# Performance work log

Hardware: AMD Instinct MI355X
Metric: run time of the kernel (lower is better)

Reference implementation:

```python
import jax, jax.numpy as jnp
import numpy as np

BS, DEC, IN_LEN, HID, EMB, VOCAB = 16, 100, 512, 768, 768, 32000


def setup_inputs() -> dict:
    key = jax.random.key(0)
    ks = jax.random.split(key, 8)
    x = jax.random.normal(ks[0], (BS, DEC, HID), dtype=jnp.float32)
    attn_dist = jax.random.normal(ks[1], (BS, DEC, IN_LEN), dtype=jnp.float32)
    enc_input = jax.random.randint(ks[2], (BS, IN_LEN), 0, VOCAB, dtype=jnp.int32)
    enc_output = jax.random.normal(ks[3], (BS, IN_LEN, EMB), dtype=jnp.float32)
    # learned params
    W_vocab = jax.random.normal(ks[4], (HID, VOCAB), dtype=jnp.float32) / np.sqrt(HID)
    b_vocab = jnp.zeros((VOCAB,), dtype=jnp.float32)
    W_gen = jax.random.normal(ks[5], (HID + EMB, 1), dtype=jnp.float32) / np.sqrt(HID + EMB)
    b_gen = jnp.zeros((1,), dtype=jnp.float32)
    return {"x": x, "attn_dist": attn_dist, "enc_input": enc_input,
            "enc_output": enc_output, "W_vocab": W_vocab, "b_vocab": b_vocab,
            "W_gen": W_gen, "b_gen": b_gen}


def reference(x, attn_dist, enc_input, enc_output, W_vocab, b_vocab, W_gen, b_gen):
    # context vector: [bs, dec, emb] = attn @ enc_output
    context = jnp.einsum('bdl,ble->bde', attn_dist, enc_output)
    mix = jnp.concatenate([context, x], axis=2)              # [bs, dec, emb+hid]
    p_gen = jax.nn.sigmoid(mix @ W_gen + b_gen)              # [bs, dec, 1]
    logit = x @ W_vocab + b_vocab                            # [bs, dec, vocab]
    vocab_dist = jax.nn.softmax(logit, axis=2) * p_gen       # [bs, dec, vocab]
    attn_w = jax.nn.softmax(attn_dist, axis=2) * (1.0 - p_gen)  # [bs, dec, in_len]
    # scatter_add attention mass onto vocab ids (duplicate ids accumulate)
    b_idx = jnp.arange(BS)[:, None, None]
    d_idx = jnp.arange(DEC)[None, :, None]
    v_idx = enc_input[:, None, :]                            # broadcast over dec
    mixed = vocab_dist.at[b_idx, d_idx, v_idx].add(attn_w)
    return jnp.log(mixed)
```

## Files before the change

kernel.cpp:

```cpp
#include <hip/hip_runtime.h>
#include <math.h>

#define BS 16
#define DEC 100
#define IN_LEN 512
#define HID 768
#define EMB 768
#define VOCAB 32000
#define NROW (BS*DEC)
#define NTILE_M 13
#define NTILE_N2 125
#define KT2 24
#define A_SHORTS 4096
#define B_SHORTS 8192

using short8 = __attribute__((ext_vector_type(8))) short;
using ushort4v = __attribute__((ext_vector_type(4))) unsigned short;
using f32x4 = __attribute__((ext_vector_type(4))) float;

__device__ __forceinline__ unsigned short f2bf(float f) {
  unsigned u = __float_as_uint(f);
  u = u + 0x7FFFu + ((u >> 16) & 1u);
  return (unsigned short)(u >> 16);
}
__device__ __forceinline__ float bf2f(unsigned short h) {
  return __uint_as_float(((unsigned)h) << 16);
}

__device__ __forceinline__ void gll16(const void* g, void* l) {
  __builtin_amdgcn_global_load_lds(
      (const __attribute__((address_space(1))) unsigned int*)g,
      (__attribute__((address_space(3))) unsigned int*)l, 16, 0, 0);
}

__global__ __launch_bounds__(256) void k0_venc(const float* __restrict__ enc_out,
                                               const float* __restrict__ Wg,
                                               float* __restrict__ venc) {
  int row = blockIdx.x * 4 + (threadIdx.x >> 6);
  int lane = threadIdx.x & 63;
  const float* p = enc_out + (size_t)row * EMB;
  float s = 0.f;
  for (int e = lane; e < EMB; e += 64) s += p[e] * Wg[e];
  for (int off = 32; off; off >>= 1) s += __shfl_xor(s, off);
  if (lane == 0) venc[row] = s;
}

__global__ __launch_bounds__(256) void k1_row(const float* __restrict__ attn,
                                              const float* __restrict__ x,
                                              const float* __restrict__ venc,
                                              const float* __restrict__ Wg,
                                              const float* __restrict__ bgen,
                                              float* __restrict__ pg,
                                              float* __restrict__ lp,
                                              float* __restrict__ m_a,
                                              float* __restrict__ s_a) {
  int r = blockIdx.x;
  int b = r / DEC;
  int tid = threadIdx.x;
  const float* arow = attn + (size_t)r * IN_LEN;
  const float* ve = venc + b * IN_LEN;
  const float* xrow = x + (size_t)r * HID;

  float pdot = 0.f, m = -1e30f;
  for (int l = tid; l < IN_LEN; l += 256) { float a = arow[l]; pdot += a * ve[l]; m = fmaxf(m, a); }
  for (int h = tid; h < HID; h += 256) pdot += xrow[h] * Wg[HID + h];

  for (int off = 32; off; off >>= 1) pdot += __shfl_xor(pdot, off);
  for (int off = 32; off; off >>= 1) m = fmaxf(m, __shfl_xor(m, off));

  __shared__ float red[8];
  if ((tid & 63) == 0) { red[tid >> 6] = pdot; red[4 + (tid >> 6)] = m; }
  __syncthreads();
  float z = red[0] + red[1] + red[2] + red[3];
  m = fmaxf(fmaxf(red[4], red[5]), fmaxf(red[6], red[7]));

  float se = 0.f;
  for (int l = tid; l < IN_LEN; l += 256) se += expf(arow[l] - m);
  for (int off = 32; off; off >>= 1) se += __shfl_xor(se, off);
  __syncthreads();
  if ((tid & 63) == 0) red[tid >> 6] = se;
  __syncthreads();
  se = red[0] + red[1] + red[2] + red[3];

  if (tid == 0) {
    z += bgen[0];
    float p, l_p;
    if (z >= 0.f) { float e = expf(-z); p = 1.f / (1.f + e); l_p = -log1pf(e); }
    else          { float e = expf(z);  p = e / (1.f + e);   l_p = z - log1pf(e); }
    pg[r] = p; lp[r] = l_p; m_a[r] = m; s_a[r] = se;
  }
}

__global__ __launch_bounds__(256) void p0_pack_x(const float* __restrict__ X,
                                                 unsigned short* __restrict__ Xp) {
  int mtile = blockIdx.x, ks = blockIdx.y, tid = threadIdx.x;
  size_t base = ((size_t)(mtile * KT2 + ks)) * A_SHORTS;
#pragma unroll
  for (int i = 0; i < 2; i++) {
    int slot = tid + i * 256;
    int r = slot >> 2, s = slot & 3;
    int row = mtile * 128 + r;
    int k0 = ks * 32 + ((s ^ (r & 3)) << 3);
    short8 v;
    if (row < NROW) {
      const float* p = X + (size_t)row * HID + k0;
#pragma unroll
      for (int j = 0; j < 8; j++) v[j] = (short)f2bf(p[j]);
    } else {
#pragma unroll
      for (int j = 0; j < 8; j++) v[j] = 0;
    }
    *(short8*)&Xp[base + (size_t)slot * 8] = v;
  }
}

__global__ __launch_bounds__(256) void p0_pack_w(const float* __restrict__ W,
                                                 unsigned short* __restrict__ Wp) {
  __shared__ float ld[32][257];
  int ntile = blockIdx.x, ks = blockIdx.y, tid = threadIdx.x;
#pragma unroll
  for (int i = 0; i < 32; i++) {
    int idx = tid + i * 256;
    int kk = idx >> 8, nn = idx & 255;
    ld[kk][nn] = W[(size_t)(ks * 32 + kk) * VOCAB + ntile * 256 + nn];
  }
  __syncthreads();
  size_t base = ((size_t)(ntile * KT2 + ks)) * B_SHORTS;
#pragma unroll
  for (int i = 0; i < 4; i++) {
    int slot = tid + i * 256;
    int n = slot >> 2, s = slot & 3;
    int k0 = (s ^ (n & 3)) << 3;
    short8 v;
#pragma unroll
    for (int j = 0; j < 8; j++) v[j] = (short)f2bf(ld[k0 + j][n]);
    *(short8*)&Wp[base + (size_t)slot * 8] = v;
  }
}

__global__ __launch_bounds__(256, 2) void k2_gemm_v4(const unsigned short* __restrict__ Xp,
                                                     const unsigned short* __restrict__ Wp,
                                                     const float* __restrict__ bvocab,
                                                     float* __restrict__ out,
                                                     unsigned short* __restrict__ lbf,
                                                     float* __restrict__ part,
                                                     int use_bf) {
  __shared__ __align__(16) unsigned short sh[3][12288];

  int bid = blockIdx.x;
  const int NWG = NTILE_M * NTILE_N2;
  const int q = NWG / 8, rr = NWG % 8;
  int xcd = bid & 7, idx = bid >> 3;
  int wg = (xcd < rr ? xcd * (q + 1) : rr * (q + 1) + (xcd - rr) * q) + idx;
  int ntile = wg / NTILE_M, mtile = wg % NTILE_M;

  const int tid = threadIdx.x;
  const int wid = tid >> 6, lane = tid & 63;
  const int wr = wid >> 1, wc = wid & 1;
  const int l15 = lane & 15, hi = lane >> 4;
  const int phys = (hi ^ (l15 & 3)) * 8;

  const unsigned short* aSrc = Xp + (size_t)(mtile * KT2) * A_SHORTS;
  const unsigned short* bSrc = Wp + (size_t)(ntile * KT2) * B_SHORTS;

  const int aoff = (wr * 64 + l15) * 32 + phys;
  const int boff = (wc * 128 + l15) * 32 + phys;

  f32x4 acc[4][8] = {};

#pragma unroll
  for (int t = 0; t < 2; t++) {
    const unsigned short* a = aSrc + (size_t)t * A_SHORTS;
    const unsigned short* b = bSrc + (size_t)t * B_SHORTS;
    unsigned short* dA = &sh[t][0];
    unsigned short* dB = &sh[t][4096];
    gll16(a + (size_t)tid * 8,            dA + tid * 8);
    gll16(a + (size_t)(tid + 256) * 8,    dA + (tid + 256) * 8);
#pragma unroll
    for (int j2 = 0; j2 < 4; j2++)
      gll16(b + (size_t)(tid + j2 * 256) * 8, dB + (tid + j2 * 256) * 8);
  }
  asm volatile("s_waitcnt vmcnt(6)" ::: "memory");
  __builtin_amdgcn_s_barrier();
  asm volatile("" ::: "memory");

  int bcur = 0;
  for (int t = 0; t < KT2; ++t) {
    if (t + 2 < KT2) {
      int bn = bcur + 2; if (bn >= 3) bn -= 3;
      const unsigned short* a = aSrc + (size_t)(t + 2) * A_SHORTS;
      const unsigned short* b = bSrc + (size_t)(t + 2) * B_SHORTS;
      unsigned short* dA = &sh[bn][0];
      unsigned short* dB = &sh[bn][4096];
      gll16(a + (size_t)tid * 8,            dA + tid * 8);
      gll16(a + (size_t)(tid + 256) * 8,    dA + (tid + 256) * 8);
#pragma unroll
      for (int j2 = 0; j2 < 4; j2++)
        gll16(b + (size_t)(tid + j2 * 256) * 8, dB + (tid + j2 * 256) * 8);
    }
    const unsigned short* A = &sh[bcur][0];
    const unsigned short* B = &sh[bcur][4096];
    short8 af[4], bfr[8];
#pragma unroll
    for (int mm = 0; mm < 4; mm++) af[mm] = *(const short8*)&A[aoff + mm * 512];
#pragma unroll
    for (int nn = 0; nn < 8; nn++) bfr[nn] = *(const short8*)&B[boff + nn * 512];
    __builtin_amdgcn_s_setprio(1);
#pragma unroll
    for (int mm = 0; mm < 4; mm++)
#pragma unroll
      for (int nn = 0; nn < 8; nn++)
        acc[mm][nn] = __builtin_amdgcn_mfma_f32_16x16x32_bf16(af[mm], bfr[nn], acc[mm][nn], 0, 0, 0);
    __builtin_amdgcn_s_setprio(0);
    if (t < KT2 - 2) { asm volatile("s_waitcnt vmcnt(6)" ::: "memory"); }
    else             { asm volatile("s_waitcnt vmcnt(0)" ::: "memory"); }
    __builtin_amdgcn_s_barrier();
    asm volatile("" ::: "memory");
    bcur = bcur + 1; if (bcur >= 3) bcur = 0;
  }

  __syncthreads();

  float bb[8];
#pragma unroll
  for (int nn = 0; nn < 8; nn++) bb[nn] = bvocab[ntile * 256 + wc * 128 + nn * 16 + l15];
#pragma unroll
  for (int mm = 0; mm < 4; mm++)
#pragma unroll
    for (int nn = 0; nn < 8; nn++)
#pragma unroll
      for (int j = 0; j < 4; j++) acc[mm][nn][j] += bb[nn];

  unsigned short* ldsC = &sh[0][0];
  float* red = (float*)&sh[2][8192];

  if (use_bf) {
#pragma unroll
    for (int mm = 0; mm < 4; mm++) {
      int row0 = wr * 64 + mm * 16 + hi * 4;
#pragma unroll
      for (int nn = 0; nn < 8; nn++) {
        int col = wc * 128 + nn * 16 + l15;
#pragma unroll
        for (int j = 0; j < 4; j++) ldsC[(row0 + j) * 256 + col] = f2bf(acc[mm][nn][j]);
      }
    }
  } else {
#pragma unroll
    for (int mm = 0; mm < 4; mm++) {
      int row0 = mtile * 128 + wr * 64 + mm * 16 + hi * 4;
#pragma unroll
      for (int nn = 0; nn < 8; nn++) {
        int col = ntile * 256 + wc * 128 + nn * 16 + l15;
#pragma unroll
        for (int j = 0; j < 4; j++) {
          int row = row0 + j;
          if (row < NROW) out[(size_t)row * VOCAB + col] = acc[mm][nn][j];
        }
      }
    }
  }

#pragma unroll
  for (int mm = 0; mm < 4; mm++) {
#pragma unroll
    for (int j = 0; j < 4; j++) {
      float mx = acc[mm][0][j];
#pragma unroll
      for (int nn = 1; nn < 8; nn++) mx = fmaxf(mx, acc[mm][nn][j]);
      mx = fmaxf(mx, __shfl_xor(mx, 1));
      mx = fmaxf(mx, __shfl_xor(mx, 2));
      mx = fmaxf(mx, __shfl_xor(mx, 4));
      mx = fmaxf(mx, __shfl_xor(mx, 8));
      float sl = 0.f;
#pragma unroll
      for (int nn = 0; nn < 8; nn++) sl += __expf(acc[mm][nn][j] - mx);
      sl += __shfl_xor(sl, 1);
      sl += __shfl_xor(sl, 2);
      sl += __shfl_xor(sl, 4);
      sl += __shfl_xor(sl, 8);
      if (l15 == 0) {
        int rloc = wr * 64 + mm * 16 + hi * 4 + j;
        int o = (rloc * 2 + wc) * 2;
        red[o] = mx; red[o + 1] = sl;
      }
    }
  }
  __syncthreads();

  if (use_bf) {
#pragma unroll
    for (int i = 0; i < 16; i++) {
      int flat = tid + i * 256;
      int r = flat >> 5, c = (flat & 31) * 8;
      int grow = mtile * 128 + r;
      if (grow < NROW)
        *(short8*)&lbf[(size_t)grow * VOCAB + ntile * 256 + c] = *(const short8*)&ldsC[r * 256 + c];
    }
  }
  if (tid < 128) {
    int o0 = (tid * 2 + 0) * 2;
    int o1 = (tid * 2 + 1) * 2;
    float m0 = red[o0], s0 = red[o0 + 1];
    float m1 = red[o1], s1 = red[o1 + 1];
    float m = fmaxf(m0, m1);
    float s = s0 * __expf(m0 - m) + s1 * __expf(m1 - m);
    int grow = mtile * 128 + tid;
    if (grow < NROW) {
      part[(size_t)grow * 256 + ntile * 2]     = m;
      part[(size_t)grow * 256 + ntile * 2 + 1] = s;
    }
  }
}

__global__ __launch_bounds__(512) void k4_fused(float* __restrict__ out,
                                                const unsigned short* __restrict__ lbf,
                                                const float* __restrict__ part,
                                                const float* __restrict__ lp,
                                                const float* __restrict__ attn,
                                                const int* __restrict__ enc,
                                                const float* __restrict__ pg,
                                                const float* __restrict__ m_a,
                                                const float* __restrict__ s_a) {
  int r = blockIdx.x >> 1;
  int half = blockIdx.x & 1;
  int tid = threadIdx.x;
  __shared__ float sm[8], ss[8], sc[1];
  __shared__ int   s_key[1024];
  __shared__ float s_val[1024];
  s_key[tid] = -1; s_key[tid + 512] = -1;
  s_val[tid] = 0.f; s_val[tid + 512] = 0.f;

  float m = -1e30f, s = 0.f;
  if (tid < NTILE_N2) {
    m = part[(size_t)r * 256 + tid * 2];
    s = part[(size_t)r * 256 + tid * 2 + 1];
  }
  for (int off = 1; off < 64; off <<= 1) {
    float mo = __shfl_xor(m, off), so = __shfl_xor(s, off);
    float nm = fmaxf(m, mo);
    s = s * __expf(m - nm) + so * __expf(mo - nm);
    m = nm;
  }
  if ((tid & 63) == 0) { sm[tid >> 6] = m; ss[tid >> 6] = s; }
  __syncthreads();
  if (tid == 0) {
    float mm_ = sm[0], ss_ = ss[0];
    for (int w = 1; w < 8; w++) {
      float nm = fmaxf(mm_, sm[w]);
      ss_ = ss_ * __expf(mm_ - nm) + ss[w] * __expf(sm[w] - nm);
      mm_ = nm;
    }
    sc[0] = lp[r] - (mm_ + __logf(ss_));
  }

  float omp = 1.f - pg[r];
  if (omp > 0.f) {
    int b_ = r / DEC;
    float t = omp * __expf(attn[(size_t)r * IN_LEN + tid] - m_a[r]) / s_a[r];
    int v = enc[b_ * IN_LEN + tid];
    int slot = v & 1023;
    while (true) {
      int old = atomicCAS(&s_key[slot], -1, v);
      if (old == -1 || old == v) { atomicAdd(&s_val[slot], t); break; }
      slot = (slot + 1) & 1023;
    }
  }
  __syncthreads();
  float coef = sc[0];

  const int HUNITS = (VOCAB / 8) / 2;
  const short8* src = (const short8*)(lbf + (size_t)r * VOCAB) + (size_t)half * HUNITS;
  float* dst = out + (size_t)r * VOCAB;
  float* dsth = dst + (size_t)half * (VOCAB / 2);
  for (int i = tid; i < HUNITS; i += 512) {
    short8 v = src[i];
    f32x4 a, b;
    a[0] = bf2f((unsigned short)v[0]) + coef; a[1] = bf2f((unsigned short)v[1]) + coef;
    a[2] = bf2f((unsigned short)v[2]) + coef; a[3] = bf2f((unsigned short)v[3]) + coef;
    b[0] = bf2f((unsigned short)v[4]) + coef; b[1] = bf2f((unsigned short)v[5]) + coef;
    b[2] = bf2f((unsigned short)v[6]) + coef; b[3] = bf2f((unsigned short)v[7]) + coef;
    __builtin_nontemporal_store(a, (f32x4*)&dsth[i * 8]);
    __builtin_nontemporal_store(b, (f32x4*)&dsth[i * 8 + 4]);
  }
  __syncthreads();

  int lo = half * (VOCAB / 2), hiR = lo + (VOCAB / 2);
  for (int i = tid; i < 1024; i += 512) {
    int v = s_key[i];
    if (v >= lo && v < hiR) {
      float sum = s_val[i];
      float p = dst[v];
      dst[v] = logf(expf(p) + sum);
    }
  }
}

__global__ __launch_bounds__(256) void k4_finish(float* __restrict__ out,
                                                 const float* __restrict__ part,
                                                 const float* __restrict__ lp) {
  int r = blockIdx.x >> 1, half = blockIdx.x & 1;
  int tid = threadIdx.x;
  float m = -1e30f, s = 0.f;
  if (tid < NTILE_N2) {
    m = part[(size_t)r * 256 + tid * 2];
    s = part[(size_t)r * 256 + tid * 2 + 1];
  }
  for (int off = 1; off < 64; off <<= 1) {
    float mo = __shfl_xor(m, off), so = __shfl_xor(s, off);
    float nm = fmaxf(m, mo);
    s = s * __expf(m - nm) + so * __expf(mo - nm);
    m = nm;
  }
  __shared__ float sm[4], ss[4], sc[1];
  if ((tid & 63) == 0) { sm[tid >> 6] = m; ss[tid >> 6] = s; }
  __syncthreads();
  if (tid == 0) {
    float mm_ = sm[0], ss_ = ss[0];
    for (int w = 1; w < 4; w++) {
      float nm = fmaxf(mm_, sm[w]);
      ss_ = ss_ * __expf(mm_ - nm) + ss[w] * __expf(sm[w] - nm);
      mm_ = nm;
    }
    sc[0] = lp[r] - (mm_ + __logf(ss_));
  }
  __syncthreads();
  float coef = sc[0];
  float4* p = (float4*)(out + (size_t)r * VOCAB + half * (VOCAB / 2));
  for (int i = tid; i < VOCAB / 8; i += 256) {
    float4 v = p[i];
    v.x += coef; v.y += coef; v.z += coef; v.w += coef;
    p[i] = v;
  }
}

__global__ __launch_bounds__(256) void k4_scatter(float* __restrict__ out,
                                                  const float* __restrict__ attn,
                                                  const int* __restrict__ enc,
                                                  const float* __restrict__ pg,
                                                  const float* __restrict__ m_a,
                                                  const float* __restrict__ s_a) {
  int idx = blockIdx.x * 256 + threadIdx.x;
  int l = idx & (IN_LEN - 1);
  int r = idx >> 9;
  int b = r / DEC;
  float omp = 1.f - pg[r];
  if (omp <= 0.f) return;
  float term = omp * expf(attn[(size_t)r * IN_LEN + l] - m_a[r]) / s_a[r];
  int v = enc[b * IN_LEN + l];
  unsigned* ua = (unsigned*)(out + (size_t)r * VOCAB + v);
  unsigned old = *ua;
  while (true) {
    float f = __uint_as_float(old);
    float nf = logf(expf(f) + term);
    unsigned assumed = old;
    old = atomicCAS(ua, assumed, __float_as_uint(nf));
    if (old == assumed) break;
  }
}

#define BM 128
#define BN 128
#define BK 32
__device__ __forceinline__ int swz_old(int row, int k) {
  int slot = (k >> 3) ^ ((row >> 1) & 3);
  return row * 32 + slot * 8 + (k & 7);
}

__global__ __launch_bounds__(256) void k2_gemm_old(const float* __restrict__ X,
                                                   const float* __restrict__ W,
                                                   const float* __restrict__ bvocab,
                                                   float* __restrict__ out) {
  __shared__ __align__(16) unsigned short As[BM * BK];
  __shared__ __align__(16) unsigned short Bs[BN * BK];
  const int mtile = blockIdx.x;
  const int ntile = blockIdx.y;
  const int tid = threadIdx.x;
  const int wid = tid >> 6, lane = tid & 63;
  const int wr = wid >> 1, wc = wid & 1;
  f32x4 acc[4][4] = {};
  float4 areg[4];
  float  breg[16];
  const int nl = tid & 127;
  const int kg = tid >> 7;
  {
#pragma unroll
    for (int i = 0; i < 4; i++) {
      int idx = tid + i * 256;
      int r = mtile * BM + (idx >> 3);
      if (r < NROW) areg[i] = *(const float4*)(X + (size_t)r * HID + (idx & 7) * 4);
      else areg[i] = make_float4(0.f, 0.f, 0.f, 0.f);
    }
    const float* base = W + (size_t)(kg * 16) * VOCAB + ntile * BN + nl;
#pragma unroll
    for (int i = 0; i < 16; i++) breg[i] = base[(size_t)i * VOCAB];
  }
  const int KS = HID / BK;
  for (int ks = 0; ks < KS; ++ks) {
#pragma unroll
    for (int i = 0; i < 4; i++) {
      int idx = tid + i * 256;
      int r = idx >> 3, kq = idx & 7;
      ushort4v w;
      w[0] = f2bf(areg[i].x); w[1] = f2bf(areg[i].y);
      w[2] = f2bf(areg[i].z); w[3] = f2bf(areg[i].w);
      *(ushort4v*)&As[swz_old(r, kq * 4)] = w;
    }
    {
      short8 v0, v1;
#pragma unroll
      for (int i = 0; i < 8; i++) { v0[i] = (short)f2bf(breg[i]); v1[i] = (short)f2bf(breg[8 + i]); }
      *(short8*)&Bs[swz_old(nl, kg * 16)] = v0;
      *(short8*)&Bs[swz_old(nl, kg * 16 + 8)] = v1;
    }
    __syncthreads();
    if (ks + 1 < KS) {
      const int ksn = ks + 1;
#pragma unroll
      for (int i = 0; i < 4; i++) {
        int idx = tid + i * 256;
        int r = mtile * BM + (idx >> 3);
        if (r < NROW) areg[i] = *(const float4*)(X + (size_t)r * HID + ksn * BK + (idx & 7) * 4);
        else areg[i] = make_float4(0.f, 0.f, 0.f, 0.f);
      }
      const float* base = W + (size_t)(ksn * BK + kg * 16) * VOCAB + ntile * BN + nl;
#pragma unroll
      for (int i = 0; i < 16; i++) breg[i] = base[(size_t)i * VOCAB];
    }
    {
      const int k0 = (lane >> 4) * 8;
      const int rbase = wr * 64 + (lane & 15);
      const int cbase = wc * 64 + (lane & 15);
      short8 af[4], bf[4];
#pragma unroll
      for (int mm = 0; mm < 4; mm++) af[mm] = *(const short8*)&As[swz_old(rbase + mm * 16, k0)];
#pragma unroll
      for (int nn = 0; nn < 4; nn++) bf[nn] = *(const short8*)&Bs[swz_old(cbase + nn * 16, k0)];
#pragma unroll
      for (int mm = 0; mm < 4; mm++)
#pragma unroll
        for (int nn = 0; nn < 4; nn++)
          acc[mm][nn] = __builtin_amdgcn_mfma_f32_16x16x32_bf16(af[mm], bf[nn], acc[mm][nn], 0, 0, 0);
    }
    __syncthreads();
  }
#pragma unroll
  for (int mm = 0; mm < 4; mm++) {
    int row0 = mtile * BM + wr * 64 + mm * 16 + (lane >> 4) * 4;
#pragma unroll
    for (int nn = 0; nn < 4; nn++) {
      int col = ntile * BN + wc * 64 + nn * 16 + (lane & 15);
      float bb = bvocab[col];
#pragma unroll
      for (int j = 0; j < 4; j++) {
        int row = row0 + j;
        if (row < NROW) out[(size_t)row * VOCAB + col] = acc[mm][nn][j] + bb;
      }
    }
  }
}

__global__ __launch_bounds__(256) void k3_norm(float* __restrict__ out,
                                               const float* __restrict__ lp) {
  int r = blockIdx.x;
  float4* row = reinterpret_cast<float4*>(out + (size_t)r * VOCAB);
  int tid = threadIdx.x;
  float m = -1e30f, s = 0.f;
  for (int i = tid; i < VOCAB / 4; i += 256) {
    float4 v = row[i];
    float m4 = fmaxf(fmaxf(v.x, v.y), fmaxf(v.z, v.w));
    if (m4 > m) { s *= __expf(m - m4); m = m4; }
    s += __expf(v.x - m) + __expf(v.y - m) + __expf(v.z - m) + __expf(v.w - m);
  }
  for (int off = 32; off; off >>= 1) {
    float mo = __shfl_xor(m, off), so = __shfl_xor(s, off);
    float nm = fmaxf(m, mo);
    s = s * __expf(m - nm) + so * __expf(mo - nm);
    m = nm;
  }
  __shared__ float mred[4], sred[4];
  if ((tid & 63) == 0) { mred[tid >> 6] = m; sred[tid >> 6] = s; }
  __syncthreads();
  if (tid == 0) {
    float mm = mred[0], ss = sred[0];
    for (int w = 1; w < 4; w++) {
      float mo = mred[w], so = sred[w];
      float nm = fmaxf(mm, mo);
      ss = ss * __expf(mm - nm) + so * __expf(mo - nm);
      mm = nm;
    }
    mred[0] = mm; sred[0] = ss;
  }
  __syncthreads();
  m = mred[0]; s = sred[0];
  float coef = lp[r] - (m + __logf(s));
  for (int i = tid; i < VOCAB / 4; i += 256) {
    float4 v = row[i];
    v.x += coef; v.y += coef; v.z += coef; v.w += coef;
    row[i] = v;
  }
}

extern "C" void kernel_launch(void* const* d_in, const int* in_sizes, int n_in,
                              void* d_out, int out_size, void* d_ws, size_t ws_size,
                              hipStream_t stream) {
  (void)in_sizes; (void)n_in; (void)out_size;
  const float* x       = (const float*)d_in[0];
  const float* attn    = (const float*)d_in[1];
  const int*   enc_in  = (const int*)d_in[2];
  const float* enc_out = (const float*)d_in[3];
  const float* Wv      = (const float*)d_in[4];
  const float* bv      = (const float*)d_in[5];
  const float* Wg      = (const float*)d_in[6];
  const float* bg      = (const float*)d_in[7];
  float* out = (float*)d_out;
  float* ws  = (float*)d_ws;

  float* venc = ws;
  float* pg   = ws + 8192;
  float* lp   = ws + 9792;
  float* m_a  = ws + 11392;
  float* s_a  = ws + 12992;
  float* part = ws + 14592;
  unsigned short* Xp = (unsigned short*)(ws + 814592);
  unsigned short* Wp = (unsigned short*)(ws + 1453568);
  unsigned short* Lbf = (unsigned short*)(ws + 13741568);
  const size_t NEED  = (size_t)13741568 * 4;
  const size_t NEED2 = NEED + (size_t)NROW * VOCAB * 2;

  hipLaunchKernelGGL(k0_venc, dim3(2048), dim3(256), 0, stream, enc_out, Wg, venc);
  hipLaunchKernelGGL(k1_row, dim3(NROW), dim3(256), 0, stream, attn, x, venc, Wg, bg,
                     pg, lp, m_a, s_a);

  if (ws_size >= NEED) {
    int use_bf = (ws_size >= NEED2) ? 1 : 0;
    hipLaunchKernelGGL(p0_pack_x, dim3(NTILE_M, KT2), dim3(256), 0, stream, x, Xp);
    hipLaunchKernelGGL(p0_pack_w, dim3(NTILE_N2, KT2), dim3(256), 0, stream, Wv, Wp);
    hipLaunchKernelGGL(k2_gemm_v4, dim3(NTILE_M * NTILE_N2), dim3(256), 0, stream,
                       Xp, Wp, bv, out, Lbf, part, use_bf);
    if (use_bf) {
      hipLaunchKernelGGL(k4_fused, dim3(NROW * 2), dim3(512), 0, stream,
                         out, Lbf, part, lp, attn, enc_in, pg, m_a, s_a);
    } else {
      hipLaunchKernelGGL(k4_finish, dim3(NROW * 2), dim3(256), 0, stream, out, part, lp);
      hipLaunchKernelGGL(k4_scatter, dim3((NROW * IN_LEN) / 256), dim3(256), 0, stream,
                         out, attn, enc_in, pg, m_a, s_a);
    }
  } else {
    hipLaunchKernelGGL(k2_gemm_old, dim3(NTILE_M, 250), dim3(256), 0, stream,
                       x, Wv, bv, out);
    hipLaunchKernelGGL(k3_norm, dim3(NROW), dim3(256), 0, stream, out, lp);
    hipLaunchKernelGGL(k4_scatter, dim3((NROW * IN_LEN) / 256), dim3(256), 0, stream,
                       out, attn, enc_in, pg, m_a, s_a);
  }
}
```

Baseline: 243.4 us.

## Repack operands in MFMA fragment order and load half of B directly to registers

The X and W packing kernels now write tiles in per-lane MFMA fragment order rather than XOR-swizzled rows, so each lane reads a contiguous 16-byte chunk. The GEMM keeps the A tile and half of the B tile in LDS with a double buffer instead of a triple buffer. The other half of B is loaded straight from global memory into registers one stage ahead. This cuts LDS traffic and footprint, at the cost of more registers and a shallower prefetch that may expose global load latency.

```diff
diff --git a/kernel.cpp b/kernel.cpp
--- a/kernel.cpp
+++ b/kernel.cpp
@@ -15,7 +15,6 @@
 #define B_SHORTS 8192
 
 using short8 = __attribute__((ext_vector_type(8))) short;
-using ushort4v = __attribute__((ext_vector_type(4))) unsigned short;
 using f32x4 = __attribute__((ext_vector_type(4))) float;
 
 __device__ __forceinline__ unsigned short f2bf(float f) {
@@ -97,10 +96,11 @@
   size_t base = ((size_t)(mtile * KT2 + ks)) * A_SHORTS;
 #pragma unroll
   for (int i = 0; i < 2; i++) {
-    int slot = tid + i * 256;
-    int r = slot >> 2, s = slot & 3;
-    int row = mtile * 128 + r;
-    int k0 = ks * 32 + ((s ^ (r & 3)) << 3);
+    int u = tid + i * 256;
+    int f = u >> 6, l = u & 63;
+    int wr = f >> 2, mm = f & 3;
+    int row = mtile * 128 + wr * 64 + mm * 16 + (l & 15);
+    int k0 = ks * 32 + (l >> 4) * 8;
     short8 v;
     if (row < NROW) {
       const float* p = X + (size_t)row * HID + k0;
@@ -110,7 +110,7 @@
 #pragma unroll
       for (int j = 0; j < 8; j++) v[j] = 0;
     }
-    *(short8*)&Xp[base + (size_t)slot * 8] = v;
+    *(short8*)&Xp[base + (size_t)u * 8] = v;
   }
 }
 
@@ -128,24 +128,28 @@
   size_t base = ((size_t)(ntile * KT2 + ks)) * B_SHORTS;
 #pragma unroll
   for (int i = 0; i < 4; i++) {
-    int slot = tid + i * 256;
-    int n = slot >> 2, s = slot & 3;
-    int k0 = (s ^ (n & 3)) << 3;
+    int u = tid + i * 256;
+    int f = u >> 6, l = u & 63;
+    int wc, nn;
+    if (f < 8) { wc = f >> 2; nn = f & 3; }
+    else       { wc = (f - 8) >> 2; nn = 4 + ((f - 8) & 3); }
+    int col = wc * 128 + nn * 16 + (l & 15);
+    int k0 = (l >> 4) * 8;
     short8 v;
 #pragma unroll
-    for (int j = 0; j < 8; j++) v[j] = (short)f2bf(ld[k0 + j][n]);
-    *(short8*)&Wp[base + (size_t)slot * 8] = v;
-  }
-}
-
-__global__ __launch_bounds__(256, 2) void k2_gemm_v4(const unsigned short* __restrict__ Xp,
+    for (int j = 0; j < 8; j++) v[j] = (short)f2bf(ld[k0 + j][col]);
+    *(short8*)&Wp[base + (size_t)u * 8] = v;
+  }
+}
+
+__global__ __launch_bounds__(256, 2) void k2_gemm_v6(const unsigned short* __restrict__ Xp,
                                                      const unsigned short* __restrict__ Wp,
                                                      const float* __restrict__ bvocab,
                                                      float* __restrict__ out,
                                                      unsigned short* __restrict__ lbf,
                                                      float* __restrict__ part,
                                                      int use_bf) {
-  __shared__ __align__(16) unsigned short sh[3][12288];
+  __shared__ __align__(16) unsigned short sh[33792];
 
   int bid = blockIdx.x;
   const int NWG = NTILE_M * NTILE_N2;
@@ -158,66 +162,86 @@
   const int wid = tid >> 6, lane = tid & 63;
   const int wr = wid >> 1, wc = wid & 1;
   const int l15 = lane & 15, hi = lane >> 4;
-  const int phys = (hi ^ (l15 & 3)) * 8;
 
   const unsigned short* aSrc = Xp + (size_t)(mtile * KT2) * A_SHORTS;
   const unsigned short* bSrc = Wp + (size_t)(ntile * KT2) * B_SHORTS;
-
-  const int aoff = (wr * 64 + l15) * 32 + phys;
-  const int boff = (wc * 128 + l15) * 32 + phys;
+  const unsigned short* bDir = bSrc + (8 + wc * 4) * 512 + lane * 8;
+
+  unsigned short* bufA0 = &sh[0];
+  unsigned short* bufA1 = &sh[4096];
+  unsigned short* bufB0 = &sh[8192];
+  unsigned short* bufB1 = &sh[12288];
+
+  const int aoff = (wr * 4) * 512 + lane * 8;
+  const int boff = (wc * 4) * 512 + lane * 8;
 
   f32x4 acc[4][8] = {};
-
-#pragma unroll
-  for (int t = 0; t < 2; t++) {
-    const unsigned short* a = aSrc + (size_t)t * A_SHORTS;
-    const unsigned short* b = bSrc + (size_t)t * B_SHORTS;
-    unsigned short* dA = &sh[t][0];
-    unsigned short* dB = &sh[t][4096];
-    gll16(a + (size_t)tid * 8,            dA + tid * 8);
-    gll16(a + (size_t)(tid + 256) * 8,    dA + (tid + 256) * 8);
-#pragma unroll
-    for (int j2 = 0; j2 < 4; j2++)
-      gll16(b + (size_t)(tid + j2 * 256) * 8, dB + (tid + j2 * 256) * 8);
-  }
-  asm volatile("s_waitcnt vmcnt(6)" ::: "memory");
+  short8 af[4], bl[4], rbA[4], rbB[4];
+
+#define STAGE(t, dA, dB) { \
+    const unsigned short* a_ = aSrc + (size_t)(t) * A_SHORTS; \
+    const unsigned short* b_ = bSrc + (size_t)(t) * B_SHORTS; \
+    gll16(a_ + (size_t)tid * 8,         dA + tid * 8); \
+    gll16(a_ + (size_t)(tid + 256) * 8, dA + (tid + 256) * 8); \
+    gll16(b_ + (size_t)tid * 8,         dB + tid * 8); \
+    gll16(b_ + (size_t)(tid + 256) * 8, dB + (tid + 256) * 8); }
+
+#define LOADDIR(dst, t) { \
+    const unsigned short* p_ = bDir + (size_t)(t) * B_SHORTS; \
+    _Pragma("unroll") for (int nn = 0; nn < 4; nn++) dst[nn] = *(const short8*)(p_ + nn * 512); }
+
+#define DSREAD(bA, bB) { \
+    _Pragma("unroll") for (int mm = 0; mm < 4; mm++) af[mm] = *(const short8*)&bA[aoff + mm * 512]; \
+    _Pragma("unroll") for (int nn = 0; nn < 4; nn++) bl[nn] = *(const short8*)&bB[boff + nn * 512]; }
+
+#define MFMA32(rb) { \
+    _Pragma("unroll") for (int mm = 0; mm < 4; mm++) { \
+      _Pragma("unroll") for (int nn = 0; nn < 4; nn++) \
+        acc[mm][nn] = __builtin_amdgcn_mfma_f32_16x16x32_bf16(af[mm], bl[nn], acc[mm][nn], 0, 0, 0); \
+      _Pragma("unroll") for (int nn = 0; nn < 4; nn++) \
+        acc[mm][4 + nn] = __builtin_amdgcn_mfma_f32_16x16x32_bf16(af[mm], rb[nn], acc[mm][4 + nn], 0, 0, 0); } }
+
+  STAGE(0, bufA0, bufB0);
+  LOADDIR(rbA, 0);
+  asm volatile("s_waitcnt vmcnt(4)" ::: "memory");
   __builtin_amdgcn_s_barrier();
   asm volatile("" ::: "memory");
 
-  int bcur = 0;
-  for (int t = 0; t < KT2; ++t) {
-    if (t + 2 < KT2) {
-      int bn = bcur + 2; if (bn >= 3) bn -= 3;
-      const unsigned short* a = aSrc + (size_t)(t + 2) * A_SHORTS;
-      const unsigned short* b = bSrc + (size_t)(t + 2) * B_SHORTS;
-      unsigned short* dA = &sh[bn][0];
-      unsigned short* dB = &sh[bn][4096];
-      gll16(a + (size_t)tid * 8,            dA + tid * 8);
-      gll16(a + (size_t)(tid + 256) * 8,    dA + (tid + 256) * 8);
-#pragma unroll
-      for (int j2 = 0; j2 < 4; j2++)
-        gll16(b + (size_t)(tid + j2 * 256) * 8, dB + (tid + j2 * 256) * 8);
-    }
-    const unsigned short* A = &sh[bcur][0];
-    const unsigned short* B = &sh[bcur][4096];
-    short8 af[4], bfr[8];
-#pragma unroll
-    for (int mm = 0; mm < 4; mm++) af[mm] = *(const short8*)&A[aoff + mm * 512];
-#pragma unroll
-    for (int nn = 0; nn < 8; nn++) bfr[nn] = *(const short8*)&B[boff + nn * 512];
+  for (int tt = 0; tt < 22; tt += 2) {
+    STAGE(tt + 1, bufA1, bufB1);
+    LOADDIR(rbB, tt + 1);
+    DSREAD(bufA0, bufB0);
     __builtin_amdgcn_s_setprio(1);
-#pragma unroll
-    for (int mm = 0; mm < 4; mm++)
-#pragma unroll
-      for (int nn = 0; nn < 8; nn++)
-        acc[mm][nn] = __builtin_amdgcn_mfma_f32_16x16x32_bf16(af[mm], bfr[nn], acc[mm][nn], 0, 0, 0);
+    MFMA32(rbA);
     __builtin_amdgcn_s_setprio(0);
-    if (t < KT2 - 2) { asm volatile("s_waitcnt vmcnt(6)" ::: "memory"); }
-    else             { asm volatile("s_waitcnt vmcnt(0)" ::: "memory"); }
+    asm volatile("s_waitcnt vmcnt(4)" ::: "memory");
     __builtin_amdgcn_s_barrier();
     asm volatile("" ::: "memory");
-    bcur = bcur + 1; if (bcur >= 3) bcur = 0;
-  }
+    STAGE(tt + 2, bufA0, bufB0);
+    LOADDIR(rbA, tt + 2);
+    DSREAD(bufA1, bufB1);
+    __builtin_amdgcn_s_setprio(1);
+    MFMA32(rbB);
+    __builtin_amdgcn_s_setprio(0);
+    asm volatile("s_waitcnt vmcnt(4)" ::: "memory");
+    __builtin_amdgcn_s_barrier();
+    asm volatile("" ::: "memory");
+  }
+  STAGE(23, bufA1, bufB1);
+  LOADDIR(rbB, 23);
+  DSREAD(bufA0, bufB0);
+  __builtin_amdgcn_s_setprio(1);
+  MFMA32(rbA);
+  __builtin_amdgcn_s_setprio(0);
+  asm volatile("s_waitcnt vmcnt(4)" ::: "memory");
+  __builtin_amdgcn_s_barrier();
+  asm volatile("" ::: "memory");
+  DSREAD(bufA1, bufB1);
+  MFMA32(rbB);
+#undef STAGE
+#undef LOADDIR
+#undef DSREAD
+#undef MFMA32
 
   __syncthreads();
 
@@ -231,8 +255,8 @@
 #pragma unroll
       for (int j = 0; j < 4; j++) acc[mm][nn][j] += bb[nn];
 
-  unsigned short* ldsC = &sh[0][0];
-  float* red = (float*)&sh[2][8192];
+  unsigned short* ldsC = &sh[0];
+  float* red = (float*)&sh[32768];
 
   if (use_bf) {
 #pragma unroll
@@ -501,10 +525,10 @@
     for (int i = 0; i < 4; i++) {
       int idx = tid + i * 256;
       int r = idx >> 3, kq = idx & 7;
-      ushort4v w;
-      w[0] = f2bf(areg[i].x); w[1] = f2bf(areg[i].y);
-      w[2] = f2bf(areg[i].z); w[3] = f2bf(areg[i].w);
-      *(ushort4v*)&As[swz_old(r, kq * 4)] = w;
+      unsigned short w0 = f2bf(areg[i].x), w1 = f2bf(areg[i].y);
+      unsigned short w2 = f2bf(areg[i].z), w3 = f2bf(areg[i].w);
+      unsigned short* dstp = &As[swz_old(r, kq * 4)];
+      dstp[0] = w0; dstp[1] = w1; dstp[2] = w2; dstp[3] = w3;
     }
     {
       short8 v0, v1;
@@ -636,7 +660,7 @@
     int use_bf = (ws_size >= NEED2) ? 1 : 0;
     hipLaunchKernelGGL(p0_pack_x, dim3(NTILE_M, KT2), dim3(256), 0, stream, x, Xp);
     hipLaunchKernelGGL(p0_pack_w, dim3(NTILE_N2, KT2), dim3(256), 0, stream, Wv, Wp);
-    hipLaunchKernelGGL(k2_gemm_v4, dim3(NTILE_M * NTILE_N2), dim3(256), 0, stream,
+    hipLaunchKernelGGL(k2_gemm_v6, dim3(NTILE_M * NTILE_N2), dim3(256), 0, stream,
                        Xp, Wp, bv, out, Lbf, part, use_bf);
     if (use_bf) {
       hipLaunchKernelGGL(k4_fused, dim3(NROW * 2), dim3(512), 0, stream,
```

Result: no change. 239.9 us (-1.4%).
